# Optimization experiments

Measured on AMD Instinct MI355X. Metric: run time of the kernel, lower is better.

Reference implementation:

```python
import jax, jax.numpy as jnp
import numpy as np

RADIUS = [3, 3, 4, 4]
DILATION = [1, 2, 1, 2]
N_HEAD = 4
D_K = 8
SCALE = 1.0 / np.sqrt(8.0)  # module hardcodes sqrt(8)


def _patches(a, r, d):
    # a: (b, t, c, h, w) -> (b, t, c, ls2, h, w), dilated (2r+1)x(2r+1) window,
    # zero padding (invalid positions masked separately).
    b, t, c, h, w = a.shape
    p = r * d
    ap = jnp.pad(a, ((0, 0), (0, 0), (0, 0), (p, p), (p, p)))
    ls = 2 * r + 1
    sl = [ap[..., dy * d:dy * d + h, dx * d:dx * d + w]
          for dy in range(ls) for dx in range(ls)]
    return jnp.stack(sl, axis=3)


def _valid_mask(h, w, r, d):
    # (ls2, h, w) bool: True where window position is inside the image
    m = _patches(jnp.ones((1, 1, 1, h, w)), r, d)
    return m[0, 0, 0] > 0.5


def _head_attn(q, k, v, r, d):
    # q,k,v: (b, t, c, h, w); attention over all t' frames x local window
    b, t, c, h, w = q.shape
    kp = _patches(k, r, d)        # (b, t', c, p, h, w)
    vp = _patches(v, r, d)
    valid = _valid_mask(h, w, r, d)  # (p, h, w)
    e = jnp.einsum('btchw,bscphw->btsphw', q, kp) * SCALE
    e = jnp.where(valid[None, None, None], e, -jnp.inf)  # OOB -> -inf like CUDA kernel
    e = e.reshape(b, t, t * valid.shape[0], h, w)
    attn = jax.nn.softmax(e, axis=2).reshape(b, t, t, -1, h, w)
    return jnp.einsum('btsphw,bscphw->btchw', attn, vp)


def setup_inputs() -> dict:
    key = jax.random.key(0)
    kx, kq, kk, kv, ko = jax.random.split(key, 5)
    C = 32
    std = 1.0 / np.sqrt(C)
    x = jax.random.normal(kx, (2, 5, C, 64, 64), dtype=jnp.float32)
    Wq = jax.random.normal(kq, (N_HEAD * D_K, C), dtype=jnp.float32) * std
    Wk = jax.random.normal(kk, (N_HEAD * D_K, C), dtype=jnp.float32) * std
    Wv = jax.random.normal(kv, (N_HEAD * D_K, C), dtype=jnp.float32) * std
    Wo = jax.random.normal(ko, (C, C), dtype=jnp.float32) * std
    return {"x": x, "Wq": Wq, "Wk": Wk, "Wv": Wv, "Wo": Wo}


def reference(x, Wq, Wk, Wv, Wo):
    # 1x1x1 Conv3d == per-pixel channel matmul
    q = jnp.einsum('btchw,kc->btkhw', x, Wq)
    k = jnp.einsum('btchw,kc->btkhw', x, Wk)
    v = jnp.einsum('btchw,kc->btkhw', x, Wv)
    outs = []
    for i in range(N_HEAD):
        s = slice(i * D_K, (i + 1) * D_K)
        outs.append(_head_attn(q[:, :, s], k[:, :, s], v[:, :, s],
                               RADIUS[i], DILATION[i]))
    out = jnp.concatenate(outs, axis=2)
    out = jnp.einsum('btchw,kc->btkhw', out, Wo)
    return out + x
```

## Files before the change

### kernel.cpp

```cpp
#include <hip/hip_runtime.h>
#include <stdint.h>

#define NT 5
#define NC 32
#define NH 4
#define HW 4096
#define NPIX 40960
#define QS 0.51006972789f
#define EBIAS 12.0f
#define NINF (-__builtin_inff())

typedef _Float16 half_t;
typedef half_t h2 __attribute__((ext_vector_type(2)));

static __device__ __forceinline__ h2 as_h2(uint32_t u) {
  union { uint32_t u; h2 h; } c; c.u = u; return c.h;
}
static __device__ __forceinline__ uint32_t pack_h2(float a, float b) {
  union { h2 h; uint32_t u; } c;
  c.h.x = (half_t)a; c.h.y = (half_t)b;
  return c.u;
}

#if __has_builtin(__builtin_amdgcn_exp2f)
#define EXP2(x) __builtin_amdgcn_exp2f(x)
#else
#define EXP2(x) exp2f(x)
#endif

static __device__ __forceinline__ float dot8i(const uint4& a, const uint4& b, float c) {
#if __has_builtin(__builtin_amdgcn_fdot2)
  c = __builtin_amdgcn_fdot2(as_h2(a.x), as_h2(b.x), c, false);
  c = __builtin_amdgcn_fdot2(as_h2(a.y), as_h2(b.y), c, false);
  c = __builtin_amdgcn_fdot2(as_h2(a.z), as_h2(b.z), c, false);
  c = __builtin_amdgcn_fdot2(as_h2(a.w), as_h2(b.w), c, false);
  return c;
#else
  const h2 a0 = as_h2(a.x), a1 = as_h2(a.y), a2 = as_h2(a.z), a3 = as_h2(a.w);
  const h2 b0 = as_h2(b.x), b1 = as_h2(b.y), b2 = as_h2(b.z), b3 = as_h2(b.w);
  c = fmaf((float)a0.x, (float)b0.x, c);
  c = fmaf((float)a0.y, (float)b0.y, c);
  c = fmaf((float)a1.x, (float)b1.x, c);
  c = fmaf((float)a1.y, (float)b1.y, c);
  c = fmaf((float)a2.x, (float)b2.x, c);
  c = fmaf((float)a2.y, (float)b2.y, c);
  c = fmaf((float)a3.x, (float)b3.x, c);
  c = fmaf((float)a3.y, (float)b3.y, c);
  return c;
#endif
}

__global__ __launch_bounds__(256) void qkv_kernel(
    const float* __restrict__ x,
    const float* __restrict__ Wq, const float* __restrict__ Wk,
    const float* __restrict__ Wv,
    uint2* __restrict__ qf, uint2* __restrict__ kf, uint2* __restrict__ vf)
{
  const int p   = blockIdx.x * 256 + threadIdx.x;
  const int by  = blockIdx.y;
  const int h   = by >> 1;
  const int jg  = by & 1;
  const int bt  = p >> 12;
  const int pix = p & 4095;

  const float* xp = x + (size_t)bt * (NC * HW) + pix;
  float xc[NC];
  #pragma unroll
  for (int c = 0; c < NC; ++c) xc[c] = xp[(size_t)c * HW];

  float qv[4], kv4[4], vv4[4];
  #pragma unroll
  for (int j = 0; j < 4; ++j) {
    const int o = h * 8 + jg * 4 + j;
    float aq = 0.f, ak = 0.f, av = 0.f;
    #pragma unroll
    for (int c = 0; c < NC; ++c) {
      const float xv = xc[c];
      aq = fmaf(xv, Wq[o * NC + c], aq);
      ak = fmaf(xv, Wk[o * NC + c], ak);
      av = fmaf(xv, Wv[o * NC + c], av);
    }
    qv[j] = aq * QS; kv4[j] = ak; vv4[j] = av;
  }
  const size_t base = (((size_t)bt * NH + h) * HW + pix) * 2 + jg;
  uint2 qq, kk, vv;
  qq.x = pack_h2(qv[0], qv[1]);  qq.y = pack_h2(qv[2], qv[3]);
  kk.x = pack_h2(kv4[0], kv4[1]); kk.y = pack_h2(kv4[2], kv4[3]);
  vv.x = pack_h2(vv4[0], vv4[1]); vv.y = pack_h2(vv4[2], vv4[3]);
  qf[base] = qq;
  kf[base] = kk;
  vf[base] = vv;
}

template <int R, int D>
static __device__ __forceinline__ void attn_body(
    int b, int t, int h, int s, int yb,
    const uint4* __restrict__ qf, const uint4* __restrict__ kf,
    const uint4* __restrict__ vf,
    uint4* __restrict__ pa, float* __restrict__ pl,
    uint4* __restrict__ k_lds, uint4* __restrict__ v_lds)
{
  constexpr int LS    = 2 * R + 1;
  constexpr int NROWS = 8 + 2 * R;
  const int tid  = threadIdx.x;
  const int w    = tid >> 6;
  const int lane = tid & 63;

  const int y0 = (D == 1) ? (yb * 8) : ((yb & 1) + 2 * ((yb >> 1) * 8));

  const uint4* kg = kf + (size_t)((b * NT + s) * NH + h) * HW;
  const uint4* vg = vf + (size_t)((b * NT + s) * NH + h) * HW;
  for (int idx = tid; idx < NROWS * 64; idx += 256) {
    const int r  = idx >> 6, xs = idx & 63;
    int ys = y0 + (r - R) * D;
    ys = ys < 0 ? 0 : (ys > 63 ? 63 : ys);
    const int pos = (D == 1) ? xs : ((xs & 1) * 32 + (xs >> 1));
    k_lds[r * 64 + pos] = kg[ys * 64 + xs];
    v_lds[r * 64 + pos] = vg[ys * 64 + xs];
  }
  __syncthreads();

  const int xp = lane >> 5;
  const int cb = (D == 1) ? lane : (lane & 31);
  const int x  = (D == 1) ? lane : (2 * (lane & 31) + xp);
  const int yA = y0 + 2 * w * D;
  const int yB = yA + D;
  const int pixA = yA * 64 + x, pixB = yB * 64 + x;

  const uint4* qp = qf + (size_t)((b * NT + t) * NH + h) * HW;
  const uint4 qA = qp[pixA];
  const uint4 qB = qp[pixB];

  float lA = 0.f, lB = 0.f;
  h2 aA[4], aB[4];
  const h2 z2 = { (half_t)0.f, (half_t)0.f };
  #pragma unroll
  for (int i = 0; i < 4; ++i) { aA[i] = z2; aB[i] = z2; }

  #pragma unroll 2
  for (int u = 0; u <= LS; ++u) {
    const int ykey = y0 + (2 * w + u - R) * D;
    const bool oky = (unsigned)ykey < 64u;
    const bool okA = (u < LS) && oky;
    const bool okB = (u > 0)  && oky;
    if (!(okA || okB)) continue;
    const float biA = okA ? -EBIAS : NINF;
    const float biB = okB ? -EBIAS : NINF;
    const uint4* kr = k_lds + (2 * w + u) * 64;
    const uint4* vr = v_lds + (2 * w + u) * 64;

    uint4 kbuf[2], vbuf[2];
    #pragma unroll
    for (int i = 0; i < 2; ++i) {
      const int cx = cb + i - R;
      const int cc = ((unsigned)cx < (D == 1 ? 64u : 32u)) ? cx : 0;
      const int pos = (D == 1) ? cc : (xp * 32 + cc);
      kbuf[i] = kr[pos];
      vbuf[i] = vr[pos];
    }
    #pragma unroll
    for (int i = 0; i < LS; ++i) {
      const int  cx  = cb + i - R;
      const bool okx = (unsigned)cx < (D == 1 ? 64u : 32u);
      const uint4 kk = kbuf[i & 1];
      const uint4 vv = vbuf[i & 1];
      if (i + 2 < LS) {
        const int cx2 = cb + i + 2 - R;
        const int cc2 = ((unsigned)cx2 < (D == 1 ? 64u : 32u)) ? cx2 : 0;
        const int pos2 = (D == 1) ? cc2 : (xp * 32 + cc2);
        kbuf[i & 1] = kr[pos2];
        vbuf[i & 1] = vr[pos2];
      }
      const float ciA = okx ? biA : NINF;
      const float ciB = okx ? biB : NINF;
      const float pA = EXP2(dot8i(qA, kk, ciA));
      const float pB = EXP2(dot8i(qB, kk, ciB));
      lA += pA; lB += pB;
      const half_t pAh = (half_t)pA, pBh = (half_t)pB;
      const h2 pA2 = { pAh, pAh }, pB2 = { pBh, pBh };
      const h2 w0 = as_h2(vv.x), w1 = as_h2(vv.y), w2 = as_h2(vv.z), w3 = as_h2(vv.w);
      aA[0] += pA2 * w0; aA[1] += pA2 * w1; aA[2] += pA2 * w2; aA[3] += pA2 * w3;
      aB[0] += pB2 * w0; aB[1] += pB2 * w1; aB[2] += pB2 * w2; aB[3] += pB2 * w3;
    }
  }

  const size_t plane = (size_t)(s * NH + h) * NPIX + (size_t)(b * NT + t) * HW;
  union { h2 hh[4]; uint4 u; } cA, cB;
  #pragma unroll
  for (int i = 0; i < 4; ++i) { cA.hh[i] = aA[i]; cB.hh[i] = aB[i]; }
  pa[plane + pixA] = cA.u;
  pa[plane + pixB] = cB.u;
  pl[plane + pixA] = lA;
  pl[plane + pixB] = lB;
}

__global__ __launch_bounds__(256) void attn_kernel(
    const uint4* __restrict__ qf, const uint4* __restrict__ kf,
    const uint4* __restrict__ vf, uint4* __restrict__ pa, float* __restrict__ pl)
{
  __shared__ uint4 k_lds[16 * 64];
  __shared__ uint4 v_lds[16 * 64];
  const int bid = blockIdx.x;
  int h, rest;
  if (bid < 800) { h = 2 + (bid & 1); rest = bid >> 1; }
  else           { h = ((bid - 800) & 1); rest = (bid - 800) >> 1; }
  const int yb = rest & 7; rest >>= 3;
  const int s  = rest % 5;
  const int bt = rest / 5;
  const int t = bt % NT, b = bt / NT;
  if      (h == 0) attn_body<3, 1>(b, t, 0, s, yb, qf, kf, vf, pa, pl, k_lds, v_lds);
  else if (h == 1) attn_body<3, 2>(b, t, 1, s, yb, qf, kf, vf, pa, pl, k_lds, v_lds);
  else if (h == 2) attn_body<4, 1>(b, t, 2, s, yb, qf, kf, vf, pa, pl, k_lds, v_lds);
  else             attn_body<4, 2>(b, t, 3, s, yb, qf, kf, vf, pa, pl, k_lds, v_lds);
}

__global__ __launch_bounds__(256) void proj_kernel(
    const uint4* __restrict__ pa, const float* __restrict__ pl,
    const float* __restrict__ x, const float* __restrict__ Wo,
    float* __restrict__ out)
{
  const int p   = blockIdx.x * 256 + threadIdx.x;
  const int og  = blockIdx.y;
  const int bt  = p >> 12;
  const int pix = p & 4095;

  float oc[32];
  #pragma unroll
  for (int h = 0; h < NH; ++h) {
    float a[8], l = 0.f;
    #pragma unroll
    for (int i = 0; i < 8; ++i) a[i] = 0.f;
    #pragma unroll
    for (int s = 0; s < NT; ++s) {
      const size_t plane = (size_t)(s * NH + h) * NPIX + p;
      const uint4 v = pa[plane];
      l += pl[plane];
      const h2 v0 = as_h2(v.x), v1 = as_h2(v.y), v2 = as_h2(v.z), v3 = as_h2(v.w);
      a[0] += (float)v0.x; a[1] += (float)v0.y;
      a[2] += (float)v1.x; a[3] += (float)v1.y;
      a[4] += (float)v2.x; a[5] += (float)v2.y;
      a[6] += (float)v3.x; a[7] += (float)v3.y;
    }
    const float inv = 1.0f / l;
    #pragma unroll
    for (int i = 0; i < 8; ++i) oc[h * 8 + i] = a[i] * inv;
  }

  const float* xpt = x + (size_t)bt * (NC * HW) + pix;
  float* yp = out + (size_t)bt * (NC * HW) + pix;
  #pragma unroll
  for (int oo = 0; oo < 4; ++oo) {
    const int o = og * 4 + oo;
    float acc = xpt[(size_t)o * HW];
    #pragma unroll
    for (int c = 0; c < NC; ++c)
      acc = fmaf(oc[c], Wo[o * NC + c], acc);
    yp[(size_t)o * HW] = acc;
  }
}

extern "C" void kernel_launch(void* const* d_in, const int* in_sizes, int n_in,
                              void* d_out, int out_size, void* d_ws, size_t ws_size,
                              hipStream_t stream)
{
  const float* x  = (const float*)d_in[0];
  const float* Wq = (const float*)d_in[1];
  const float* Wk = (const float*)d_in[2];
  const float* Wv = (const float*)d_in[3];
  const float* Wo = (const float*)d_in[4];

  char* ws = (char*)d_ws;
  uint2* qf = (uint2*)ws;
  uint2* kf = (uint2*)(ws + 2621440);
  uint2* vf = (uint2*)(ws + 2 * 2621440);
  uint4* pa = (uint4*)(ws + 3 * 2621440);
  float* pl = (float*)(ws + 3 * 2621440 + 13107200);

  qkv_kernel<<<dim3(160, 8), 256, 0, stream>>>(x, Wq, Wk, Wv, qf, kf, vf);
  attn_kernel<<<1600, 256, 0, stream>>>((const uint4*)qf, (const uint4*)kf,
                                        (const uint4*)vf, pa, pl);
  proj_kernel<<<dim3(160, 8), 256, 0, stream>>>(pa, pl, x, Wo, (float*)d_out);
}
```

Measured before the change: 111.7 us.

## Split radius-4 heads' key-row loop across two blocks with extra partial planes

```diff
diff --git a/kernel.cpp b/kernel.cpp
--- a/kernel.cpp
+++ b/kernel.cpp
@@ -6,6 +6,7 @@
 #define NH 4
 #define HW 4096
 #define NPIX 40960
+#define NPLANES 30
 #define QS 0.51006972789f
 #define EBIAS 12.0f
 #define NINF (-__builtin_inff())
@@ -92,16 +93,16 @@
   vf[base] = vv;
 }
 
-template <int R, int D>
+template <int R, int D, int U0, int UN>
 static __device__ __forceinline__ void attn_body(
-    int b, int t, int h, int s, int yb,
+    int b, int t, int h, int s, int yb, int plane_id,
     const uint4* __restrict__ qf, const uint4* __restrict__ kf,
     const uint4* __restrict__ vf,
     uint4* __restrict__ pa, float* __restrict__ pl,
     uint4* __restrict__ k_lds, uint4* __restrict__ v_lds)
 {
   constexpr int LS    = 2 * R + 1;
-  constexpr int NROWS = 8 + 2 * R;
+  constexpr int NROWS = UN + 6;
   const int tid  = threadIdx.x;
   const int w    = tid >> 6;
   const int lane = tid & 63;
@@ -112,7 +113,7 @@
   const uint4* vg = vf + (size_t)((b * NT + s) * NH + h) * HW;
   for (int idx = tid; idx < NROWS * 64; idx += 256) {
     const int r  = idx >> 6, xs = idx & 63;
-    int ys = y0 + (r - R) * D;
+    int ys = y0 + (r + U0 - R) * D;
     ys = ys < 0 ? 0 : (ys > 63 ? 63 : ys);
     const int pos = (D == 1) ? xs : ((xs & 1) * 32 + (xs >> 1));
     k_lds[r * 64 + pos] = kg[ys * 64 + xs];
@@ -138,7 +139,7 @@
   for (int i = 0; i < 4; ++i) { aA[i] = z2; aB[i] = z2; }
 
   #pragma unroll 2
-  for (int u = 0; u <= LS; ++u) {
+  for (int u = U0; u < U0 + UN; ++u) {
     const int ykey = y0 + (2 * w + u - R) * D;
     const bool oky = (unsigned)ykey < 64u;
     const bool okA = (u < LS) && oky;
@@ -146,8 +147,8 @@
     if (!(okA || okB)) continue;
     const float biA = okA ? -EBIAS : NINF;
     const float biB = okB ? -EBIAS : NINF;
-    const uint4* kr = k_lds + (2 * w + u) * 64;
-    const uint4* vr = v_lds + (2 * w + u) * 64;
+    const uint4* kr = k_lds + (2 * w + u - U0) * 64;
+    const uint4* vr = v_lds + (2 * w + u - U0) * 64;
 
     uint4 kbuf[2], vbuf[2];
     #pragma unroll
@@ -184,7 +185,7 @@
     }
   }
 
-  const size_t plane = (size_t)(s * NH + h) * NPIX + (size_t)(b * NT + t) * HW;
+  const size_t plane = (size_t)plane_id * NPIX + (size_t)(b * NT + t) * HW;
   union { h2 hh[4]; uint4 u; } cA, cB;
   #pragma unroll
   for (int i = 0; i < 4; ++i) { cA.hh[i] = aA[i]; cB.hh[i] = aB[i]; }
@@ -198,20 +199,27 @@
     const uint4* __restrict__ qf, const uint4* __restrict__ kf,
     const uint4* __restrict__ vf, uint4* __restrict__ pa, float* __restrict__ pl)
 {
-  __shared__ uint4 k_lds[16 * 64];
-  __shared__ uint4 v_lds[16 * 64];
+  __shared__ uint4 k_lds[14 * 64];
+  __shared__ uint4 v_lds[14 * 64];
   const int bid = blockIdx.x;
-  int h, rest;
-  if (bid < 800) { h = 2 + (bid & 1); rest = bid >> 1; }
-  else           { h = ((bid - 800) & 1); rest = (bid - 800) >> 1; }
+  int h, half, rest;
+  if (bid < 800) { h = bid & 1; half = 0; rest = bid >> 1; }
+  else { const int q = bid - 800; h = 2 + (q & 1); half = (q >> 1) & 1; rest = q >> 2; }
   const int yb = rest & 7; rest >>= 3;
   const int s  = rest % 5;
   const int bt = rest / 5;
   const int t = bt % NT, b = bt / NT;
-  if      (h == 0) attn_body<3, 1>(b, t, 0, s, yb, qf, kf, vf, pa, pl, k_lds, v_lds);
-  else if (h == 1) attn_body<3, 2>(b, t, 1, s, yb, qf, kf, vf, pa, pl, k_lds, v_lds);
-  else if (h == 2) attn_body<4, 1>(b, t, 2, s, yb, qf, kf, vf, pa, pl, k_lds, v_lds);
-  else             attn_body<4, 2>(b, t, 3, s, yb, qf, kf, vf, pa, pl, k_lds, v_lds);
+  const int pbase = s * NH + h;
+  const int psplit = 20 + s * 2 + (h - 2);
+  if      (h == 0) attn_body<3, 1, 0, 8>(b, t, 0, s, yb, pbase, qf, kf, vf, pa, pl, k_lds, v_lds);
+  else if (h == 1) attn_body<3, 2, 0, 8>(b, t, 1, s, yb, pbase, qf, kf, vf, pa, pl, k_lds, v_lds);
+  else if (h == 2) {
+    if (half == 0) attn_body<4, 1, 0, 5>(b, t, 2, s, yb, pbase,  qf, kf, vf, pa, pl, k_lds, v_lds);
+    else           attn_body<4, 1, 5, 5>(b, t, 2, s, yb, psplit, qf, kf, vf, pa, pl, k_lds, v_lds);
+  } else {
+    if (half == 0) attn_body<4, 2, 0, 5>(b, t, 3, s, yb, pbase,  qf, kf, vf, pa, pl, k_lds, v_lds);
+    else           attn_body<4, 2, 5, 5>(b, t, 3, s, yb, psplit, qf, kf, vf, pa, pl, k_lds, v_lds);
+  }
 }
 
 __global__ __launch_bounds__(256) void proj_kernel(
@@ -241,6 +249,19 @@
       a[4] += (float)v2.x; a[5] += (float)v2.y;
       a[6] += (float)v3.x; a[7] += (float)v3.y;
     }
+    if (h >= 2) {
+      #pragma unroll
+      for (int s = 0; s < NT; ++s) {
+        const size_t plane = (size_t)(20 + s * 2 + (h - 2)) * NPIX + p;
+        const uint4 v = pa[plane];
+        l += pl[plane];
+        const h2 v0 = as_h2(v.x), v1 = as_h2(v.y), v2 = as_h2(v.z), v3 = as_h2(v.w);
+        a[0] += (float)v0.x; a[1] += (float)v0.y;
+        a[2] += (float)v1.x; a[3] += (float)v1.y;
+        a[4] += (float)v2.x; a[5] += (float)v2.y;
+        a[6] += (float)v3.x; a[7] += (float)v3.y;
+      }
+    }
     const float inv = 1.0f / l;
     #pragma unroll
     for (int i = 0; i < 8; ++i) oc[h * 8 + i] = a[i] * inv;
@@ -274,10 +295,10 @@
   uint2* kf = (uint2*)(ws + 2621440);
   uint2* vf = (uint2*)(ws + 2 * 2621440);
   uint4* pa = (uint4*)(ws + 3 * 2621440);
-  float* pl = (float*)(ws + 3 * 2621440 + 13107200);
+  float* pl = (float*)(ws + 3 * 2621440 + 19660800);
 
   qkv_kernel<<<dim3(160, 8), 256, 0, stream>>>(x, Wq, Wk, Wv, qf, kf, vf);
-  attn_kernel<<<1600, 256, 0, stream>>>((const uint4*)qf, (const uint4*)kf,
+  attn_kernel<<<2400, 256, 0, stream>>>((const uint4*)qf, (const uint4*)kf,
                                         (const uint4*)vf, pa, pl);
   proj_kernel<<<dim3(160, 8), 256, 0, stream>>>(pa, pl, x, Wo, (float*)d_out);
 }
```

Result: slower. 115.7 us (+3.6%).

## Loop over source frames inside attention blocks instead of splitting across blocks

Applied to the files above, without the earlier changes.

```diff
diff --git a/kernel.cpp b/kernel.cpp
--- a/kernel.cpp
+++ b/kernel.cpp
@@ -94,10 +94,9 @@
 
 template <int R, int D>
 static __device__ __forceinline__ void attn_body(
-    int b, int t, int h, int s, int yb,
+    int b, int t, int h, int yb,
     const uint4* __restrict__ qf, const uint4* __restrict__ kf,
-    const uint4* __restrict__ vf,
-    uint4* __restrict__ pa, float* __restrict__ pl,
+    const uint4* __restrict__ vf, uint4* __restrict__ of,
     uint4* __restrict__ k_lds, uint4* __restrict__ v_lds)
 {
   constexpr int LS    = 2 * R + 1;
@@ -107,18 +106,6 @@
   const int lane = tid & 63;
 
   const int y0 = (D == 1) ? (yb * 8) : ((yb & 1) + 2 * ((yb >> 1) * 8));
-
-  const uint4* kg = kf + (size_t)((b * NT + s) * NH + h) * HW;
-  const uint4* vg = vf + (size_t)((b * NT + s) * NH + h) * HW;
-  for (int idx = tid; idx < NROWS * 64; idx += 256) {
-    const int r  = idx >> 6, xs = idx & 63;
-    int ys = y0 + (r - R) * D;
-    ys = ys < 0 ? 0 : (ys > 63 ? 63 : ys);
-    const int pos = (D == 1) ? xs : ((xs & 1) * 32 + (xs >> 1));
-    k_lds[r * 64 + pos] = kg[ys * 64 + xs];
-    v_lds[r * 64 + pos] = vg[ys * 64 + xs];
-  }
-  __syncthreads();
 
   const int xp = lane >> 5;
   const int cb = (D == 1) ? lane : (lane & 31);
@@ -131,93 +118,123 @@
   const uint4 qA = qp[pixA];
   const uint4 qB = qp[pixB];
 
-  float lA = 0.f, lB = 0.f;
-  h2 aA[4], aB[4];
-  const h2 z2 = { (half_t)0.f, (half_t)0.f };
-  #pragma unroll
-  for (int i = 0; i < 4; ++i) { aA[i] = z2; aB[i] = z2; }
-
-  #pragma unroll 2
-  for (int u = 0; u <= LS; ++u) {
-    const int ykey = y0 + (2 * w + u - R) * D;
-    const bool oky = (unsigned)ykey < 64u;
-    const bool okA = (u < LS) && oky;
-    const bool okB = (u > 0)  && oky;
-    if (!(okA || okB)) continue;
-    const float biA = okA ? -EBIAS : NINF;
-    const float biB = okB ? -EBIAS : NINF;
-    const uint4* kr = k_lds + (2 * w + u) * 64;
-    const uint4* vr = v_lds + (2 * w + u) * 64;
-
-    uint4 kbuf[2], vbuf[2];
-    #pragma unroll
-    for (int i = 0; i < 2; ++i) {
-      const int cx = cb + i - R;
-      const int cc = ((unsigned)cx < (D == 1 ? 64u : 32u)) ? cx : 0;
-      const int pos = (D == 1) ? cc : (xp * 32 + cc);
-      kbuf[i] = kr[pos];
-      vbuf[i] = vr[pos];
-    }
-    #pragma unroll
-    for (int i = 0; i < LS; ++i) {
-      const int  cx  = cb + i - R;
-      const bool okx = (unsigned)cx < (D == 1 ? 64u : 32u);
-      const uint4 kk = kbuf[i & 1];
-      const uint4 vv = vbuf[i & 1];
-      if (i + 2 < LS) {
-        const int cx2 = cb + i + 2 - R;
-        const int cc2 = ((unsigned)cx2 < (D == 1 ? 64u : 32u)) ? cx2 : 0;
-        const int pos2 = (D == 1) ? cc2 : (xp * 32 + cc2);
-        kbuf[i & 1] = kr[pos2];
-        vbuf[i & 1] = vr[pos2];
+  float lAt = 0.f, lBt = 0.f;
+  float oA[8], oB[8];
+  #pragma unroll
+  for (int i = 0; i < 8; ++i) { oA[i] = 0.f; oB[i] = 0.f; }
+
+  for (int s = 0; s < NT; ++s) {
+    const uint4* kg = kf + (size_t)((b * NT + s) * NH + h) * HW;
+    const uint4* vg = vf + (size_t)((b * NT + s) * NH + h) * HW;
+    __syncthreads();
+    for (int idx = tid; idx < NROWS * 64; idx += 256) {
+      const int r  = idx >> 6, xs = idx & 63;
+      int ys = y0 + (r - R) * D;
+      ys = ys < 0 ? 0 : (ys > 63 ? 63 : ys);
+      const int pos = (D == 1) ? xs : ((xs & 1) * 32 + (xs >> 1));
+      k_lds[r * 64 + pos] = kg[ys * 64 + xs];
+      v_lds[r * 64 + pos] = vg[ys * 64 + xs];
+    }
+    __syncthreads();
+
+    float lA = 0.f, lB = 0.f;
+    h2 aA[4], aB[4];
+    const h2 z2 = { (half_t)0.f, (half_t)0.f };
+    #pragma unroll
+    for (int i = 0; i < 4; ++i) { aA[i] = z2; aB[i] = z2; }
+
+    #pragma unroll 2
+    for (int u = 0; u <= LS; ++u) {
+      const int ykey = y0 + (2 * w + u - R) * D;
+      const bool oky = (unsigned)ykey < 64u;
+      const bool okA = (u < LS) && oky;
+      const bool okB = (u > 0)  && oky;
+      if (!(okA || okB)) continue;
+      const float biA = okA ? -EBIAS : NINF;
+      const float biB = okB ? -EBIAS : NINF;
+      const uint4* kr = k_lds + (2 * w + u) * 64;
+      const uint4* vr = v_lds + (2 * w + u) * 64;
+
+      uint4 kbuf[2], vbuf[2];
+      #pragma unroll
+      for (int i = 0; i < 2; ++i) {
+        const int cx = cb + i - R;
+        const int cc = ((unsigned)cx < (D == 1 ? 64u : 32u)) ? cx : 0;
+        const int pos = (D == 1) ? cc : (xp * 32 + cc);
+        kbuf[i] = kr[pos];
+        vbuf[i] = vr[pos];
       }
-      const float ciA = okx ? biA : NINF;
-      const float ciB = okx ? biB : NINF;
-      const float pA = EXP2(dot8i(qA, kk, ciA));
-      const float pB = EXP2(dot8i(qB, kk, ciB));
-      lA += pA; lB += pB;
-      const half_t pAh = (half_t)pA, pBh = (half_t)pB;
-      const h2 pA2 = { pAh, pAh }, pB2 = { pBh, pBh };
-      const h2 w0 = as_h2(vv.x), w1 = as_h2(vv.y), w2 = as_h2(vv.z), w3 = as_h2(vv.w);
-      aA[0] += pA2 * w0; aA[1] += pA2 * w1; aA[2] += pA2 * w2; aA[3] += pA2 * w3;
-      aB[0] += pB2 * w0; aB[1] += pB2 * w1; aB[2] += pB2 * w2; aB[3] += pB2 * w3;
-    }
-  }
-
-  const size_t plane = (size_t)(s * NH + h) * NPIX + (size_t)(b * NT + t) * HW;
-  union { h2 hh[4]; uint4 u; } cA, cB;
-  #pragma unroll
-  for (int i = 0; i < 4; ++i) { cA.hh[i] = aA[i]; cB.hh[i] = aB[i]; }
-  pa[plane + pixA] = cA.u;
-  pa[plane + pixB] = cB.u;
-  pl[plane + pixA] = lA;
-  pl[plane + pixB] = lB;
+      #pragma unroll
+      for (int i = 0; i < LS; ++i) {
+        const int  cx  = cb + i - R;
+        const bool okx = (unsigned)cx < (D == 1 ? 64u : 32u);
+        const uint4 kk = kbuf[i & 1];
+        const uint4 vv = vbuf[i & 1];
+        if (i + 2 < LS) {
+          const int cx2 = cb + i + 2 - R;
+          const int cc2 = ((unsigned)cx2 < (D == 1 ? 64u : 32u)) ? cx2 : 0;
+          const int pos2 = (D == 1) ? cc2 : (xp * 32 + cc2);
+          kbuf[i & 1] = kr[pos2];
+          vbuf[i & 1] = vr[pos2];
+        }
+        const float ciA = okx ? biA : NINF;
+        const float ciB = okx ? biB : NINF;
+        const float pA = EXP2(dot8i(qA, kk, ciA));
+        const float pB = EXP2(dot8i(qB, kk, ciB));
+        lA += pA; lB += pB;
+        const half_t pAh = (half_t)pA, pBh = (half_t)pB;
+        const h2 pA2 = { pAh, pAh }, pB2 = { pBh, pBh };
+        const h2 w0 = as_h2(vv.x), w1 = as_h2(vv.y), w2 = as_h2(vv.z), w3 = as_h2(vv.w);
+        aA[0] += pA2 * w0; aA[1] += pA2 * w1; aA[2] += pA2 * w2; aA[3] += pA2 * w3;
+        aB[0] += pB2 * w0; aB[1] += pB2 * w1; aB[2] += pB2 * w2; aB[3] += pB2 * w3;
+      }
+    }
+
+    lAt += lA; lBt += lB;
+    #pragma unroll
+    for (int i = 0; i < 4; ++i) {
+      oA[2 * i]     += (float)aA[i].x; oA[2 * i + 1] += (float)aA[i].y;
+      oB[2 * i]     += (float)aB[i].x; oB[2 * i + 1] += (float)aB[i].y;
+    }
+  }
+
+  const float invA = 1.0f / lAt, invB = 1.0f / lBt;
+  uint4 rA, rB;
+  rA.x = pack_h2(oA[0] * invA, oA[1] * invA);
+  rA.y = pack_h2(oA[2] * invA, oA[3] * invA);
+  rA.z = pack_h2(oA[4] * invA, oA[5] * invA);
+  rA.w = pack_h2(oA[6] * invA, oA[7] * invA);
+  rB.x = pack_h2(oB[0] * invB, oB[1] * invB);
+  rB.y = pack_h2(oB[2] * invB, oB[3] * invB);
+  rB.z = pack_h2(oB[4] * invB, oB[5] * invB);
+  rB.w = pack_h2(oB[6] * invB, oB[7] * invB);
+  const size_t plane = (size_t)h * NPIX + (size_t)(b * NT + t) * HW;
+  of[plane + pixA] = rA;
+  of[plane + pixB] = rB;
 }
 
 __global__ __launch_bounds__(256) void attn_kernel(
     const uint4* __restrict__ qf, const uint4* __restrict__ kf,
-    const uint4* __restrict__ vf, uint4* __restrict__ pa, float* __restrict__ pl)
+    const uint4* __restrict__ vf, uint4* __restrict__ of)
 {
   __shared__ uint4 k_lds[16 * 64];
   __shared__ uint4 v_lds[16 * 64];
   const int bid = blockIdx.x;
   int h, rest;
-  if (bid < 800) { h = 2 + (bid & 1); rest = bid >> 1; }
-  else           { h = ((bid - 800) & 1); rest = (bid - 800) >> 1; }
-  const int yb = rest & 7; rest >>= 3;
-  const int s  = rest % 5;
-  const int bt = rest / 5;
+  if (bid < 160) { h = 2 + (bid & 1); rest = bid >> 1; }
+  else           { h = ((bid - 160) & 1); rest = (bid - 160) >> 1; }
+  const int yb = rest & 7;
+  const int bt = rest >> 3;
   const int t = bt % NT, b = bt / NT;
-  if      (h == 0) attn_body<3, 1>(b, t, 0, s, yb, qf, kf, vf, pa, pl, k_lds, v_lds);
-  else if (h == 1) attn_body<3, 2>(b, t, 1, s, yb, qf, kf, vf, pa, pl, k_lds, v_lds);
-  else if (h == 2) attn_body<4, 1>(b, t, 2, s, yb, qf, kf, vf, pa, pl, k_lds, v_lds);
-  else             attn_body<4, 2>(b, t, 3, s, yb, qf, kf, vf, pa, pl, k_lds, v_lds);
+  if      (h == 0) attn_body<3, 1>(b, t, 0, yb, qf, kf, vf, of, k_lds, v_lds);
+  else if (h == 1) attn_body<3, 2>(b, t, 1, yb, qf, kf, vf, of, k_lds, v_lds);
+  else if (h == 2) attn_body<4, 1>(b, t, 2, yb, qf, kf, vf, of, k_lds, v_lds);
+  else             attn_body<4, 2>(b, t, 3, yb, qf, kf, vf, of, k_lds, v_lds);
 }
 
 __global__ __launch_bounds__(256) void proj_kernel(
-    const uint4* __restrict__ pa, const float* __restrict__ pl,
-    const float* __restrict__ x, const float* __restrict__ Wo,
-    float* __restrict__ out)
+    const uint4* __restrict__ of, const float* __restrict__ x,
+    const float* __restrict__ Wo, float* __restrict__ out)
 {
   const int p   = blockIdx.x * 256 + threadIdx.x;
   const int og  = blockIdx.y;
@@ -227,23 +244,12 @@
   float oc[32];
   #pragma unroll
   for (int h = 0; h < NH; ++h) {
-    float a[8], l = 0.f;
-    #pragma unroll
-    for (int i = 0; i < 8; ++i) a[i] = 0.f;
-    #pragma unroll
-    for (int s = 0; s < NT; ++s) {
-      const size_t plane = (size_t)(s * NH + h) * NPIX + p;
-      const uint4 v = pa[plane];
-      l += pl[plane];
-      const h2 v0 = as_h2(v.x), v1 = as_h2(v.y), v2 = as_h2(v.z), v3 = as_h2(v.w);
-      a[0] += (float)v0.x; a[1] += (float)v0.y;
-      a[2] += (float)v1.x; a[3] += (float)v1.y;
-      a[4] += (float)v2.x; a[5] += (float)v2.y;
-      a[6] += (float)v3.x; a[7] += (float)v3.y;
-    }
-    const float inv = 1.0f / l;
-    #pragma unroll
-    for (int i = 0; i < 8; ++i) oc[h * 8 + i] = a[i] * inv;
+    const uint4 v = of[(size_t)h * NPIX + p];
+    const h2 v0 = as_h2(v.x), v1 = as_h2(v.y), v2 = as_h2(v.z), v3 = as_h2(v.w);
+    oc[h * 8 + 0] = (float)v0.x; oc[h * 8 + 1] = (float)v0.y;
+    oc[h * 8 + 2] = (float)v1.x; oc[h * 8 + 3] = (float)v1.y;
+    oc[h * 8 + 4] = (float)v2.x; oc[h * 8 + 5] = (float)v2.y;
+    oc[h * 8 + 6] = (float)v3.x; oc[h * 8 + 7] = (float)v3.y;
   }
 
   const float* xpt = x + (size_t)bt * (NC * HW) + pix;
@@ -273,11 +279,11 @@
   uint2* qf = (uint2*)ws;
   uint2* kf = (uint2*)(ws + 2621440);
   uint2* vf = (uint2*)(ws + 2 * 2621440);
-  uint4* pa = (uint4*)(ws + 3 * 2621440);
-  float* pl = (float*)(ws + 3 * 2621440 + 13107200);
+  uint4* of = (uint4*)(ws + 3 * 2621440);
 
   qkv_kernel<<<dim3(160, 8), 256, 0, stream>>>(x, Wq, Wk, Wv, qf, kf, vf);
-  attn_kernel<<<1600, 256, 0, stream>>>((const uint4*)qf, (const uint4*)kf,
-                                        (const uint4*)vf, pa, pl);
-  proj_kernel<<<dim3(160, 8), 256, 0, stream>>>(pa, pl, x, Wo, (float*)d_out);
-}
+  attn_kernel<<<320, 256, 0, stream>>>((const uint4*)qf, (const uint4*)kf,
+                                       (const uint4*)vf, of);
+  proj_kernel<<<dim3(160, 8), 256, 0, stream>>>((const uint4*)of, x, Wo,
+                                                (float*)d_out);
+}
```

Measured after the change: 121.5 us. +8.7%, slower.
